# Kernel optimization log

Measured on AMD Instinct MI355X. Metric: run time of the kernel, lower is better.

## Reference

```python
import jax, jax.numpy as jnp
import numpy as np

EPS = 0.5  # energy-relaxation learning rate (epsilon in __init__)


def rho(s):
    return jnp.clip(s, 0.0, 1.0)


def setup_inputs() -> dict:
    key = jax.random.key(0)
    k_x, k_w1, k_w2 = jax.random.split(key, 3)
    B, I, H, O = 8192, 1024, 128, 1000
    x = jax.random.uniform(k_x, (B, I), dtype=jnp.float32)
    hidden0 = jnp.zeros((B, H), dtype=jnp.float32)
    output0 = jnp.zeros((B, O), dtype=jnp.float32)
    b_in = jnp.zeros((I,), dtype=jnp.float32)
    b_h = jnp.zeros((H,), dtype=jnp.float32)
    b_o = jnp.zeros((O,), dtype=jnp.float32)
    # xavier_uniform: U(-a, a), a = sqrt(6 / (fan_in + fan_out))
    a1 = np.sqrt(6.0 / (I + H)).astype(np.float32)
    a2 = np.sqrt(6.0 / (H + O)).astype(np.float32)
    W1 = jax.random.uniform(k_w1, (I, H), minval=-a1, maxval=a1, dtype=jnp.float32)
    W2 = jax.random.uniform(k_w2, (H, O), minval=-a2, maxval=a2, dtype=jnp.float32)
    return {"x": x, "hidden0": hidden0, "output0": output0,
            "b_in": b_in, "b_h": b_h, "b_o": b_o,
            "W1": W1, "W2": W2, "n_iterations": 30}


def reference(x, hidden0, output0, b_in, b_h, b_o, W1, W2, n_iterations):
    # Hopfield-style energy summed over the batch (beta=0 / free phase):
    # E = 0.5*sum rho(s)^2 - sum rho(s).b - sum rho(pre) W rho(post)
    def energy(h, o):
        rx, rh, ro = rho(x), rho(h), rho(o)
        sq = 0.5 * ((rx * rx).sum() + (rh * rh).sum() + (ro * ro).sum())
        lin = -(rx @ b_in).sum() - (rh @ b_h).sum() - (ro @ b_o).sum()
        quad = -jnp.einsum('bi,ih,bh->', rx, W1, rh) \
               - jnp.einsum('bh,ho,bo->', rh, W2, ro)
        return sq + lin + quad

    grad_e = jax.grad(energy, argnums=(0, 1))

    def step(carry, _):
        h, o = carry
        gh, go = grad_e(h, o)
        h = jnp.clip(h - EPS * gh, 0.0, 1.0)
        o = jnp.clip(o - EPS * go, 0.0, 1.0)
        return (h, o), None

    (h, o), _ = jax.lax.scan(step, (hidden0, output0), None, length=n_iterations)
    return jax.nn.log_softmax(o, axis=1)
```

## Files before the change

### kernel.cpp

```cpp
#include <hip/hip_runtime.h>
#include <hip/hip_bf16.h>

typedef __bf16 bf16_t;
typedef __bf16 bf16x4_t __attribute__((ext_vector_type(4)));
typedef __bf16 bf16x8 __attribute__((ext_vector_type(8)));
typedef float f32x16 __attribute__((ext_vector_type(16)));

#define EPS 0.5f
#define MFMA32(a, b, c) __builtin_amdgcn_mfma_f32_32x32x16_bf16(a, b, c, 0, 0, 0)

__device__ __forceinline__ int oswz(int row, int kbyte) {
  return (row << 11) + (kbyte ^ ((row & 15) << 4));
}
__device__ __forceinline__ int hswz(int row, int jbyte) {
  return (row << 8) + (jbyte ^ ((row & 15) << 4));
}

__global__ __launch_bounds__(256) void prep_weights(
    const float* __restrict__ W1, const float* __restrict__ W2,
    bf16_t* __restrict__ W1t, bf16_t* __restrict__ W2B, bf16_t* __restrict__ W2T) {
  int idx = blockIdx.x * 256 + threadIdx.x;
  if (idx < 131072) {
    { int j = idx >> 10, i = idx & 1023; W1t[idx] = (bf16_t)W1[i * 128 + j]; }
    { int e = idx & 7, l = (idx >> 3) & 63, s = (idx >> 9) & 63, jt = idx >> 15;
      int j = jt * 32 + (l & 31), k = s * 16 + (l >> 5) * 8 + e;
      W2B[idx] = (bf16_t)((k < 1000) ? W2[j * 1000 + k] : 0.f); }
    { int e = idx & 7, l = (idx >> 3) & 63, js = (idx >> 9) & 7, kt = idx >> 12;
      int k = kt * 32 + (l & 31), j = js * 16 + (l >> 5) * 8 + e;
      W2T[idx] = (bf16_t)((k < 1000) ? W2[j * 1000 + k] : 0.f); }
  }
}

__global__ __launch_bounds__(256) void gemm_A(
    const float* __restrict__ x, const bf16_t* __restrict__ W1t,
    float* __restrict__ A) {
  int lane = threadIdx.x & 63, w = threadIdx.x >> 6;
  int row0 = blockIdx.x * 64;
  int mt = w & 1, np = (w >> 1) * 2;
  f32x16 acc0 = {}, acc1 = {};
  int ar = row0 + mt * 32 + (lane & 31);
  int kg = (lane >> 5) * 8;
  const float* xrow = x + (size_t)ar * 1024 + kg;
  const bf16_t* b0 = W1t + ((np * 32 + (lane & 31)) << 10) + kg;
  const bf16_t* b1 = W1t + (((np + 1) * 32 + (lane & 31)) << 10) + kg;
#pragma unroll 4
  for (int ks = 0; ks < 64; ++ks) {
    float xv[8];
    *(float4*)&xv[0] = *(const float4*)(xrow + ks * 16);
    *(float4*)&xv[4] = *(const float4*)(xrow + ks * 16 + 4);
    bf16x8 a;
#pragma unroll
    for (int i = 0; i < 8; ++i) a[i] = (bf16_t)xv[i];
    bf16x8 f0 = *(const bf16x8*)(b0 + ks * 16);
    bf16x8 f1 = *(const bf16x8*)(b1 + ks * 16);
    acc0 = MFMA32(a, f0, acc0);
    acc1 = MFMA32(a, f1, acc1);
  }
#pragma unroll
  for (int reg = 0; reg < 16; ++reg) {
    int r = mt * 32 + (reg & 3) + 8 * (reg >> 2) + 4 * (lane >> 5);
    A[(size_t)(row0 + r) * 128 + np * 32 + (lane & 31)] = acc0[reg];
    A[(size_t)(row0 + r) * 128 + (np + 1) * 32 + (lane & 31)] = acc1[reg];
  }
}

__global__ __launch_bounds__(1024, 4) void eqprop(
    const float* __restrict__ h0, const float* __restrict__ o0,
    const float* __restrict__ b_h, const float* __restrict__ b_o,
    const float* __restrict__ A, const bf16_t* __restrict__ W2B,
    const bf16_t* __restrict__ W2T, const int* __restrict__ nit,
    float* __restrict__ out) {
  __shared__ __align__(16) char ob[2][65536];
  __shared__ __align__(16) char hb[2][8192];
  __shared__ float bo_lds[1024];

  const int tid = threadIdx.x, lane = tid & 63, w = tid >> 6;
  const int lo = lane & 31, hi = lane >> 5;
  const int row0 = blockIdx.x * 32;

  for (int idx = tid; idx < 8192; idx += 1024) {
    int r = idx >> 8, k4 = (idx & 255) * 4;
    bf16x4_t v4 = {};
    if (k4 < 1000) {
      float4 v = *(const float4*)(o0 + (size_t)(row0 + r) * 1000 + k4);
      v4[0] = (bf16_t)v.x; v4[1] = (bf16_t)v.y; v4[2] = (bf16_t)v.z; v4[3] = (bf16_t)v.w;
    }
    *(bf16x4_t*)(&ob[0][0] + oswz(r, k4 * 2)) = v4;
  }
  {
    int idx = tid;
    if (idx < 1024) {
      int r = idx >> 5, j4 = (idx & 31) * 4;
      float4 v = *(const float4*)(h0 + (size_t)(row0 + r) * 128 + j4);
      bf16x4_t v4;
      v4[0] = (bf16_t)v.x; v4[1] = (bf16_t)v.y; v4[2] = (bf16_t)v.z; v4[3] = (bf16_t)v.w;
      *(bf16x4_t*)(&hb[0][0] + hswz(r, j4 * 2)) = v4;
    }
  }
  bo_lds[tid] = (tid < 1000) ? b_o[tid] : 0.f;

  const int T = nit[0];
  int p = 0;
  __syncthreads();

  if (w < 4) {
    const int jt = w;
    const bf16_t* WB = W2B + (size_t)jt * 64 * 512 + lane * 8;
    bf16x8 wres[16];
#pragma unroll
    for (int s = 0; s < 16; ++s) wres[s] = *(const bf16x8*)(WB + s * 512);
    const bf16_t* WS = WB + 16 * 512;

    for (int t = 0; t < T; ++t) {
      const char* op = &ob[p][0];
      f32x16 acc = {};
#pragma unroll
      for (int s = 0; s < 16; ++s) {
        bf16x8 of = *(const bf16x8*)(op + oswz(lo, s * 32 + hi * 16));
        acc = MFMA32(wres[s], of, acc);
      }
#pragma unroll 1
      for (int c = 0; c < 12; ++c) {
        bf16x8 w0 = *(const bf16x8*)(WS + (c * 4 + 0) * 512);
        bf16x8 w1 = *(const bf16x8*)(WS + (c * 4 + 1) * 512);
        bf16x8 w2 = *(const bf16x8*)(WS + (c * 4 + 2) * 512);
        bf16x8 w3 = *(const bf16x8*)(WS + (c * 4 + 3) * 512);
        int s0 = (16 + c * 4) * 32 + hi * 16;
        bf16x8 f0 = *(const bf16x8*)(op + oswz(lo, s0));
        bf16x8 f1 = *(const bf16x8*)(op + oswz(lo, s0 + 32));
        bf16x8 f2 = *(const bf16x8*)(op + oswz(lo, s0 + 64));
        bf16x8 f3 = *(const bf16x8*)(op + oswz(lo, s0 + 96));
        acc = MFMA32(w0, f0, acc);
        acc = MFMA32(w1, f1, acc);
        acc = MFMA32(w2, f2, acc);
        acc = MFMA32(w3, f3, acc);
      }
      const char* hp = &hb[p][0];
      char* hn = &hb[p ^ 1][0];
#pragma unroll
      for (int q = 0; q < 4; ++q) {
        int jb = jt * 32 + q * 8 + 4 * hi;
        float av[4], bh[4];
        *(float4*)av = *(const float4*)(A + (size_t)(row0 + lo) * 128 + jb);
        *(float4*)bh = *(const float4*)(b_h + jb);
        bf16x4_t hv4 = *(const bf16x4_t*)(hp + hswz(lo, jb * 2));
        bf16x4_t hn4;
#pragma unroll
        for (int r = 0; r < 4; ++r) {
          float hv = (float)hv4[r];
          float rp = (hv == 0.f || hv == 1.f) ? 0.5f : 1.f;
          float nv = hv - EPS * rp * (hv - bh[r] - av[r] - acc[q * 4 + r]);
          hn4[r] = (bf16_t)fminf(fmaxf(nv, 0.f), 1.f);
        }
        *(bf16x4_t*)(hn + hswz(lo, jb * 2)) = hn4;
      }
      __syncthreads();
      p ^= 1;
    }
  } else {
    const int wd = w - 4;
    const int kt0 = (wd < 8) ? wd * 3 : 24 + (wd - 8) * 2;
    const int nkt = (wd < 8) ? 3 : 2;
    const bf16_t* WT = W2T + (size_t)kt0 * 8 * 512 + lane * 8;
    bf16x8 wres[12];
#pragma unroll
    for (int f = 0; f < 12; ++f) wres[f] = *(const bf16x8*)(WT + f * 512);

    for (int t = 0; t < T; ++t) {
      const char* hp = &hb[p][0];
      const char* op = &ob[p][0];
      char* on = &ob[p ^ 1][0];

#pragma unroll 1
      for (int kl = 0; kl < nkt; ++kl) {
        f32x16 acc = {};
        if (kl == 0) {
#pragma unroll
          for (int js = 0; js < 8; ++js) {
            bf16x8 hf = *(const bf16x8*)(hp + hswz(lo, js * 32 + hi * 16));
            acc = MFMA32(wres[js], hf, acc);
          }
        } else if (kl == 1) {
          bf16x8 s0 = *(const bf16x8*)(WT + 12 * 512);
          bf16x8 s1 = *(const bf16x8*)(WT + 13 * 512);
          bf16x8 s2 = *(const bf16x8*)(WT + 14 * 512);
          bf16x8 s3 = *(const bf16x8*)(WT + 15 * 512);
#pragma unroll
          for (int js = 0; js < 4; ++js) {
            bf16x8 hf = *(const bf16x8*)(hp + hswz(lo, js * 32 + hi * 16));
            acc = MFMA32(wres[8 + js], hf, acc);
          }
          {
            bf16x8 h4 = *(const bf16x8*)(hp + hswz(lo, 4 * 32 + hi * 16));
            bf16x8 h5 = *(const bf16x8*)(hp + hswz(lo, 5 * 32 + hi * 16));
            bf16x8 h6 = *(const bf16x8*)(hp + hswz(lo, 6 * 32 + hi * 16));
            bf16x8 h7 = *(const bf16x8*)(hp + hswz(lo, 7 * 32 + hi * 16));
            acc = MFMA32(s0, h4, acc);
            acc = MFMA32(s1, h5, acc);
            acc = MFMA32(s2, h6, acc);
            acc = MFMA32(s3, h7, acc);
          }
        } else {
          const bf16_t* WK = WT + 16 * 512;
          bf16x8 s0 = *(const bf16x8*)(WK + 0 * 512);
          bf16x8 s1 = *(const bf16x8*)(WK + 1 * 512);
          bf16x8 s2 = *(const bf16x8*)(WK + 2 * 512);
          bf16x8 s3 = *(const bf16x8*)(WK + 3 * 512);
#pragma unroll
          for (int js = 0; js < 4; ++js) {
            bf16x8 hf = *(const bf16x8*)(hp + hswz(lo, js * 32 + hi * 16));
            acc = MFMA32((js == 0) ? s0 : (js == 1) ? s1 : (js == 2) ? s2 : s3,
                         hf, acc);
          }
          bf16x8 s4 = *(const bf16x8*)(WK + 4 * 512);
          bf16x8 s5 = *(const bf16x8*)(WK + 5 * 512);
          bf16x8 s6 = *(const bf16x8*)(WK + 6 * 512);
          bf16x8 s7 = *(const bf16x8*)(WK + 7 * 512);
#pragma unroll
          for (int js = 4; js < 8; ++js) {
            bf16x8 hf = *(const bf16x8*)(hp + hswz(lo, js * 32 + hi * 16));
            acc = MFMA32((js == 4) ? s4 : (js == 5) ? s5 : (js == 6) ? s6 : s7,
                         hf, acc);
          }
        }
        int kt = kt0 + kl;
#pragma unroll
        for (int q = 0; q < 4; ++q) {
          int kb = kt * 32 + q * 8 + 4 * hi;
          float bo[4];
          *(float4*)bo = *(const float4*)(bo_lds + kb);
          bf16x4_t ov4 = *(const bf16x4_t*)(op + oswz(lo, kb * 2));
          bf16x4_t on4;
#pragma unroll
          for (int r = 0; r < 4; ++r) {
            float ov = (float)ov4[r];
            float rp = (ov == 0.f || ov == 1.f) ? 0.5f : 1.f;
            float nv = ov - EPS * rp * (ov - bo[r] - acc[q * 4 + r]);
            on4[r] = (bf16_t)fminf(fmaxf(nv, 0.f), 1.f);
          }
          *(bf16x4_t*)(on + oswz(lo, kb * 2)) = on4;
        }
      }
      __syncthreads();
      p ^= 1;
    }
  }
  __syncthreads();

  const char* of = &ob[p][0];
  for (int r = w * 2; r < w * 2 + 2; ++r) {
    float m = -1e30f;
    for (int k = lane; k < 1000; k += 64)
      m = fmaxf(m, (float)*(const bf16_t*)(of + oswz(r, k * 2)));
#pragma unroll
    for (int s = 32; s > 0; s >>= 1) m = fmaxf(m, __shfl_xor(m, s));
    float sum = 0.f;
    for (int k = lane; k < 1000; k += 64)
      sum += expf((float)*(const bf16_t*)(of + oswz(r, k * 2)) - m);
#pragma unroll
    for (int s = 32; s > 0; s >>= 1) sum += __shfl_xor(sum, s);
    float lse = m + logf(sum);
    for (int k = lane; k < 1000; k += 64)
      out[(size_t)(row0 + r) * 1000 + k] =
          (float)*(const bf16_t*)(of + oswz(r, k * 2)) - lse;
  }
}

extern "C" void kernel_launch(void* const* d_in, const int* in_sizes, int n_in,
                              void* d_out, int out_size, void* d_ws, size_t ws_size,
                              hipStream_t stream) {
  const float* x   = (const float*)d_in[0];
  const float* h0  = (const float*)d_in[1];
  const float* o0  = (const float*)d_in[2];
  const float* b_h = (const float*)d_in[4];
  const float* b_o = (const float*)d_in[5];
  const float* W1  = (const float*)d_in[6];
  const float* W2  = (const float*)d_in[7];
  const int*   nit = (const int*)d_in[8];
  float* out = (float*)d_out;

  char* ws = (char*)d_ws;
  float*  A   = (float*)ws;
  bf16_t* W1t = (bf16_t*)(ws + 4194304);
  bf16_t* W2B = (bf16_t*)(ws + 4194304 + 262144);
  bf16_t* W2T = (bf16_t*)(ws + 4194304 + 524288);

  prep_weights<<<512, 256, 0, stream>>>(W1, W2, W1t, W2B, W2T);
  gemm_A<<<128, 256, 0, stream>>>(x, W1t, A);
  eqprop<<<256, 1024, 0, stream>>>(h0, o0, b_h, b_o, A, W2B, W2T, nit, out);
}
```

Baseline: 227.0 us.

## Repack LDS state into MFMA-fragment layout and rebalance waves to 768 threads

Replaces the XOR-swizzled row-major LDS buffers for the output and hidden states with a layout that matches the MFMA fragment order, so each lane reads a contiguous 16-byte fragment with a simple offset. The output-update waves drop from 12 to 8, each owning 4 k-tiles with software-pipelined (double-buffered) streaming weight loads, and the block size drops from 1024 to 768. The A+b_h term is hoisted out of the iteration loop into registers, and the update math is rewritten with FMAs. The risks are higher register pressure per wave, fewer waves to hide latency, and a slower scalar-by-scalar initial fill of LDS.

```diff
diff --git a/kernel.cpp b/kernel.cpp
--- a/kernel.cpp
+++ b/kernel.cpp
@@ -8,13 +8,6 @@
 
 #define EPS 0.5f
 #define MFMA32(a, b, c) __builtin_amdgcn_mfma_f32_32x32x16_bf16(a, b, c, 0, 0, 0)
-
-__device__ __forceinline__ int oswz(int row, int kbyte) {
-  return (row << 11) + (kbyte ^ ((row & 15) << 4));
-}
-__device__ __forceinline__ int hswz(int row, int jbyte) {
-  return (row << 8) + (jbyte ^ ((row & 15) << 4));
-}
 
 __global__ __launch_bounds__(256) void prep_weights(
     const float* __restrict__ W1, const float* __restrict__ W2,
@@ -64,40 +57,33 @@
   }
 }
 
-__global__ __launch_bounds__(1024, 4) void eqprop(
+__global__ __launch_bounds__(768, 3) void eqprop(
     const float* __restrict__ h0, const float* __restrict__ o0,
     const float* __restrict__ b_h, const float* __restrict__ b_o,
     const float* __restrict__ A, const bf16_t* __restrict__ W2B,
     const bf16_t* __restrict__ W2T, const int* __restrict__ nit,
     float* __restrict__ out) {
-  __shared__ __align__(16) char ob[2][65536];
-  __shared__ __align__(16) char hb[2][8192];
+  __shared__ __align__(16) char o_raw[131072];
+  __shared__ __align__(16) char h_raw[16384];
   __shared__ float bo_lds[1024];
 
   const int tid = threadIdx.x, lane = tid & 63, w = tid >> 6;
   const int lo = lane & 31, hi = lane >> 5;
   const int row0 = blockIdx.x * 32;
 
-  for (int idx = tid; idx < 8192; idx += 1024) {
-    int r = idx >> 8, k4 = (idx & 255) * 4;
-    bf16x4_t v4 = {};
-    if (k4 < 1000) {
-      float4 v = *(const float4*)(o0 + (size_t)(row0 + r) * 1000 + k4);
-      v4[0] = (bf16_t)v.x; v4[1] = (bf16_t)v.y; v4[2] = (bf16_t)v.z; v4[3] = (bf16_t)v.w;
-    }
-    *(bf16x4_t*)(&ob[0][0] + oswz(r, k4 * 2)) = v4;
-  }
-  {
-    int idx = tid;
-    if (idx < 1024) {
-      int r = idx >> 5, j4 = (idx & 31) * 4;
-      float4 v = *(const float4*)(h0 + (size_t)(row0 + r) * 128 + j4);
-      bf16x4_t v4;
-      v4[0] = (bf16_t)v.x; v4[1] = (bf16_t)v.y; v4[2] = (bf16_t)v.z; v4[3] = (bf16_t)v.w;
-      *(bf16x4_t*)(&hb[0][0] + hswz(r, j4 * 2)) = v4;
-    }
-  }
-  bo_lds[tid] = (tid < 1000) ? b_o[tid] : 0.f;
+  for (int idx = tid; idx < 32768; idx += 768) {
+    int b = idx >> 10, k = idx & 1023;
+    float v = (k < 1000) ? o0[(size_t)(row0 + b) * 1000 + k] : 0.f;
+    int ad = ((k >> 4) << 10) + ((((k >> 3) & 1) << 5) + b) * 16 + ((k & 7) << 1);
+    *(bf16_t*)(o_raw + ad) = (bf16_t)v;
+  }
+  for (int idx = tid; idx < 4096; idx += 768) {
+    int b = idx >> 7, j = idx & 127;
+    int ad = ((j >> 4) << 10) + ((((j >> 3) & 1) << 5) + b) * 16 + ((j & 7) << 1);
+    *(bf16_t*)(h_raw + ad) = (bf16_t)h0[(size_t)(row0 + b) * 128 + j];
+  }
+  for (int idx = tid; idx < 1024; idx += 768)
+    bo_lds[idx] = (idx < 1000) ? b_o[idx] : 0.f;
 
   const int T = nit[0];
   int p = 0;
@@ -105,164 +91,173 @@
 
   if (w < 4) {
     const int jt = w;
-    const bf16_t* WB = W2B + (size_t)jt * 64 * 512 + lane * 8;
+    const bf16_t* WB = W2B + (size_t)jt * 32768 + lane * 8;
+#define CW(s) (*(const bf16x8*)(WB + (s) * 512))
     bf16x8 wres[16];
 #pragma unroll
-    for (int s = 0; s < 16; ++s) wres[s] = *(const bf16x8*)(WB + s * 512);
-    const bf16_t* WS = WB + 16 * 512;
+    for (int s = 0; s < 16; ++s) wres[s] = CW(s);
+    float uh[16];
+#pragma unroll
+    for (int q = 0; q < 4; ++q) {
+      int jb = jt * 32 + q * 8 + 4 * hi;
+      float4 a4 = *(const float4*)(A + (size_t)(row0 + lo) * 128 + jb);
+      float4 b4 = *(const float4*)(b_h + jb);
+      uh[q * 4 + 0] = a4.x + b4.x; uh[q * 4 + 1] = a4.y + b4.y;
+      uh[q * 4 + 2] = a4.z + b4.z; uh[q * 4 + 3] = a4.w + b4.w;
+    }
+    const char* obase = o_raw + lane * 16;
+    const char* hrd_b = h_raw + lo * 16 + hi * 8;
+    char* hwr_b = h_raw + lo * 16 + hi * 8;
 
     for (int t = 0; t < T; ++t) {
-      const char* op = &ob[p][0];
+      const char* obP = obase + (p << 16);
+#define OF(s) (*(const bf16x8*)(obP + (s) * 1024))
       f32x16 acc = {};
 #pragma unroll
-      for (int s = 0; s < 16; ++s) {
-        bf16x8 of = *(const bf16x8*)(op + oswz(lo, s * 32 + hi * 16));
-        acc = MFMA32(wres[s], of, acc);
+      for (int s = 0; s < 16; ++s) acc = MFMA32(wres[s], OF(s), acc);
+      bf16x8 cs0[4], cs1[4];
+      cs0[0] = CW(16); cs0[1] = CW(17); cs0[2] = CW(18); cs0[3] = CW(19);
+#pragma unroll
+      for (int c = 0; c < 12; ++c) {
+        const int s0 = 16 + c * 4;
+        if ((c & 1) == 0) {
+          if (c < 11) {
+            cs1[0] = CW(s0 + 4); cs1[1] = CW(s0 + 5);
+            cs1[2] = CW(s0 + 6); cs1[3] = CW(s0 + 7);
+          }
+          acc = MFMA32(cs0[0], OF(s0 + 0), acc);
+          acc = MFMA32(cs0[1], OF(s0 + 1), acc);
+          acc = MFMA32(cs0[2], OF(s0 + 2), acc);
+          acc = MFMA32(cs0[3], OF(s0 + 3), acc);
+        } else {
+          if (c < 11) {
+            cs0[0] = CW(s0 + 4); cs0[1] = CW(s0 + 5);
+            cs0[2] = CW(s0 + 6); cs0[3] = CW(s0 + 7);
+          }
+          acc = MFMA32(cs1[0], OF(s0 + 0), acc);
+          acc = MFMA32(cs1[1], OF(s0 + 1), acc);
+          acc = MFMA32(cs1[2], OF(s0 + 2), acc);
+          acc = MFMA32(cs1[3], OF(s0 + 3), acc);
+        }
       }
-#pragma unroll 1
-      for (int c = 0; c < 12; ++c) {
-        bf16x8 w0 = *(const bf16x8*)(WS + (c * 4 + 0) * 512);
-        bf16x8 w1 = *(const bf16x8*)(WS + (c * 4 + 1) * 512);
-        bf16x8 w2 = *(const bf16x8*)(WS + (c * 4 + 2) * 512);
-        bf16x8 w3 = *(const bf16x8*)(WS + (c * 4 + 3) * 512);
-        int s0 = (16 + c * 4) * 32 + hi * 16;
-        bf16x8 f0 = *(const bf16x8*)(op + oswz(lo, s0));
-        bf16x8 f1 = *(const bf16x8*)(op + oswz(lo, s0 + 32));
-        bf16x8 f2 = *(const bf16x8*)(op + oswz(lo, s0 + 64));
-        bf16x8 f3 = *(const bf16x8*)(op + oswz(lo, s0 + 96));
-        acc = MFMA32(w0, f0, acc);
-        acc = MFMA32(w1, f1, acc);
-        acc = MFMA32(w2, f2, acc);
-        acc = MFMA32(w3, f3, acc);
-      }
-      const char* hp = &hb[p][0];
-      char* hn = &hb[p ^ 1][0];
+      const char* hrd = hrd_b + (p << 13);
+      char* hwr = hwr_b + ((p ^ 1) << 13);
 #pragma unroll
       for (int q = 0; q < 4; ++q) {
-        int jb = jt * 32 + q * 8 + 4 * hi;
-        float av[4], bh[4];
-        *(float4*)av = *(const float4*)(A + (size_t)(row0 + lo) * 128 + jb);
-        *(float4*)bh = *(const float4*)(b_h + jb);
-        bf16x4_t hv4 = *(const bf16x4_t*)(hp + hswz(lo, jb * 2));
+        const int boff = (jt * 2 + (q >> 1)) * 1024 + (q & 1) * 512;
+        bf16x4_t hv4 = *(const bf16x4_t*)(hrd + boff);
         bf16x4_t hn4;
 #pragma unroll
         for (int r = 0; r < 4; ++r) {
           float hv = (float)hv4[r];
-          float rp = (hv == 0.f || hv == 1.f) ? 0.5f : 1.f;
-          float nv = hv - EPS * rp * (hv - bh[r] - av[r] - acc[q * 4 + r]);
+          float tie = __builtin_fmaf(hv, hv, -hv);
+          float st = (tie == 0.f) ? 0.25f : 0.5f;
+          float nv = __builtin_fmaf(-st, hv - uh[q * 4 + r] - acc[q * 4 + r], hv);
           hn4[r] = (bf16_t)fminf(fmaxf(nv, 0.f), 1.f);
         }
-        *(bf16x4_t*)(hn + hswz(lo, jb * 2)) = hn4;
+        *(bf16x4_t*)(hwr + boff) = hn4;
       }
       __syncthreads();
       p ^= 1;
     }
   } else {
-    const int wd = w - 4;
-    const int kt0 = (wd < 8) ? wd * 3 : 24 + (wd - 8) * 2;
-    const int nkt = (wd < 8) ? 3 : 2;
-    const bf16_t* WT = W2T + (size_t)kt0 * 8 * 512 + lane * 8;
-    bf16x8 wres[12];
-#pragma unroll
-    for (int f = 0; f < 12; ++f) wres[f] = *(const bf16x8*)(WT + f * 512);
+    const int wd4 = (w - 4) * 4;
+    const bf16_t* WT = W2T + lane * 8;
+#define DW(kt, js) (*(const bf16x8*)(WT + (size_t)((kt) * 8 + (js)) * 512))
+#define DLOAD(dst, kt) { dst[0] = DW(kt, 4); dst[1] = DW(kt, 5); \
+                         dst[2] = DW(kt, 6); dst[3] = DW(kt, 7); }
+    bf16x8 wr[4][4];
+#pragma unroll
+    for (int i = 0; i < 4; ++i)
+#pragma unroll
+      for (int js = 0; js < 4; ++js) wr[i][js] = DW(wd4 + i, js);
+
+    const char* hbase = h_raw + lane * 16;
+    const char* ord_b = o_raw + lo * 16 + hi * 8;
+    char* owr_b = o_raw + lo * 16 + hi * 8;
 
     for (int t = 0; t < T; ++t) {
-      const char* hp = &hb[p][0];
-      const char* op = &ob[p][0];
-      char* on = &ob[p ^ 1][0];
-
-#pragma unroll 1
-      for (int kl = 0; kl < nkt; ++kl) {
+      const char* hbP = hbase + (p << 13);
+      bf16x8 hf[8];
+#pragma unroll
+      for (int js = 0; js < 8; ++js)
+        hf[js] = *(const bf16x8*)(hbP + js * 1024);
+      const char* ord = ord_b + (p << 16);
+      char* owr = owr_b + ((p ^ 1) << 16);
+
+      bf16x8 sw0[4], sw1[4];
+      DLOAD(sw0, wd4);
+#pragma unroll
+      for (int i = 0; i < 4; ++i) {
+        const int kt = wd4 + i;
         f32x16 acc = {};
-        if (kl == 0) {
-#pragma unroll
-          for (int js = 0; js < 8; ++js) {
-            bf16x8 hf = *(const bf16x8*)(hp + hswz(lo, js * 32 + hi * 16));
-            acc = MFMA32(wres[js], hf, acc);
-          }
-        } else if (kl == 1) {
-          bf16x8 s0 = *(const bf16x8*)(WT + 12 * 512);
-          bf16x8 s1 = *(const bf16x8*)(WT + 13 * 512);
-          bf16x8 s2 = *(const bf16x8*)(WT + 14 * 512);
-          bf16x8 s3 = *(const bf16x8*)(WT + 15 * 512);
-#pragma unroll
-          for (int js = 0; js < 4; ++js) {
-            bf16x8 hf = *(const bf16x8*)(hp + hswz(lo, js * 32 + hi * 16));
-            acc = MFMA32(wres[8 + js], hf, acc);
-          }
-          {
-            bf16x8 h4 = *(const bf16x8*)(hp + hswz(lo, 4 * 32 + hi * 16));
-            bf16x8 h5 = *(const bf16x8*)(hp + hswz(lo, 5 * 32 + hi * 16));
-            bf16x8 h6 = *(const bf16x8*)(hp + hswz(lo, 6 * 32 + hi * 16));
-            bf16x8 h7 = *(const bf16x8*)(hp + hswz(lo, 7 * 32 + hi * 16));
-            acc = MFMA32(s0, h4, acc);
-            acc = MFMA32(s1, h5, acc);
-            acc = MFMA32(s2, h6, acc);
-            acc = MFMA32(s3, h7, acc);
-          }
+        if ((i & 1) == 0) {
+          if (i < 3) DLOAD(sw1, kt + 1);
+          acc = MFMA32(wr[i][0], hf[0], acc);
+          acc = MFMA32(wr[i][1], hf[1], acc);
+          acc = MFMA32(wr[i][2], hf[2], acc);
+          acc = MFMA32(wr[i][3], hf[3], acc);
+          acc = MFMA32(sw0[0], hf[4], acc);
+          acc = MFMA32(sw0[1], hf[5], acc);
+          acc = MFMA32(sw0[2], hf[6], acc);
+          acc = MFMA32(sw0[3], hf[7], acc);
         } else {
-          const bf16_t* WK = WT + 16 * 512;
-          bf16x8 s0 = *(const bf16x8*)(WK + 0 * 512);
-          bf16x8 s1 = *(const bf16x8*)(WK + 1 * 512);
-          bf16x8 s2 = *(const bf16x8*)(WK + 2 * 512);
-          bf16x8 s3 = *(const bf16x8*)(WK + 3 * 512);
-#pragma unroll
-          for (int js = 0; js < 4; ++js) {
-            bf16x8 hf = *(const bf16x8*)(hp + hswz(lo, js * 32 + hi * 16));
-            acc = MFMA32((js == 0) ? s0 : (js == 1) ? s1 : (js == 2) ? s2 : s3,
-                         hf, acc);
-          }
-          bf16x8 s4 = *(const bf16x8*)(WK + 4 * 512);
-          bf16x8 s5 = *(const bf16x8*)(WK + 5 * 512);
-          bf16x8 s6 = *(const bf16x8*)(WK + 6 * 512);
-          bf16x8 s7 = *(const bf16x8*)(WK + 7 * 512);
-#pragma unroll
-          for (int js = 4; js < 8; ++js) {
-            bf16x8 hf = *(const bf16x8*)(hp + hswz(lo, js * 32 + hi * 16));
-            acc = MFMA32((js == 4) ? s4 : (js == 5) ? s5 : (js == 6) ? s6 : s7,
-                         hf, acc);
-          }
-        }
-        int kt = kt0 + kl;
+          if (i < 3) DLOAD(sw0, kt + 1);
+          acc = MFMA32(wr[i][0], hf[0], acc);
+          acc = MFMA32(wr[i][1], hf[1], acc);
+          acc = MFMA32(wr[i][2], hf[2], acc);
+          acc = MFMA32(wr[i][3], hf[3], acc);
+          acc = MFMA32(sw1[0], hf[4], acc);
+          acc = MFMA32(sw1[1], hf[5], acc);
+          acc = MFMA32(sw1[2], hf[6], acc);
+          acc = MFMA32(sw1[3], hf[7], acc);
+        }
 #pragma unroll
         for (int q = 0; q < 4; ++q) {
-          int kb = kt * 32 + q * 8 + 4 * hi;
-          float bo[4];
-          *(float4*)bo = *(const float4*)(bo_lds + kb);
-          bf16x4_t ov4 = *(const bf16x4_t*)(op + oswz(lo, kb * 2));
+          const int boff = (kt * 2 + (q >> 1)) * 1024 + (q & 1) * 512;
+          float bov[4];
+          *(float4*)bov = *(const float4*)(bo_lds + kt * 32 + q * 8 + 4 * hi);
+          bf16x4_t ov4 = *(const bf16x4_t*)(ord + boff);
           bf16x4_t on4;
 #pragma unroll
           for (int r = 0; r < 4; ++r) {
             float ov = (float)ov4[r];
-            float rp = (ov == 0.f || ov == 1.f) ? 0.5f : 1.f;
-            float nv = ov - EPS * rp * (ov - bo[r] - acc[q * 4 + r]);
+            float u = bov[r] + acc[q * 4 + r];
+            float tie = __builtin_fmaf(ov, ov, -ov);
+            float st = (tie == 0.f) ? 0.25f : 0.5f;
+            float nv = __builtin_fmaf(-st, ov - u, ov);
             on4[r] = (bf16_t)fminf(fmaxf(nv, 0.f), 1.f);
           }
-          *(bf16x4_t*)(on + oswz(lo, kb * 2)) = on4;
+          *(bf16x4_t*)(owr + boff) = on4;
         }
       }
       __syncthreads();
       p ^= 1;
     }
   }
-  __syncthreads();
-
-  const char* of = &ob[p][0];
-  for (int r = w * 2; r < w * 2 + 2; ++r) {
+
+  const char* of = o_raw + (p << 16);
+  for (int row = w; row < 32; row += 12) {
     float m = -1e30f;
-    for (int k = lane; k < 1000; k += 64)
-      m = fmaxf(m, (float)*(const bf16_t*)(of + oswz(r, k * 2)));
+    for (int k = lane; k < 1000; k += 64) {
+      int ad = ((k >> 4) << 10) + ((((k >> 3) & 1) << 5) + row) * 16 + ((k & 7) << 1);
+      m = fmaxf(m, (float)*(const bf16_t*)(of + ad));
+    }
 #pragma unroll
     for (int s = 32; s > 0; s >>= 1) m = fmaxf(m, __shfl_xor(m, s));
     float sum = 0.f;
-    for (int k = lane; k < 1000; k += 64)
-      sum += expf((float)*(const bf16_t*)(of + oswz(r, k * 2)) - m);
+    for (int k = lane; k < 1000; k += 64) {
+      int ad = ((k >> 4) << 10) + ((((k >> 3) & 1) << 5) + row) * 16 + ((k & 7) << 1);
+      sum += expf((float)*(const bf16_t*)(of + ad) - m);
+    }
 #pragma unroll
     for (int s = 32; s > 0; s >>= 1) sum += __shfl_xor(sum, s);
     float lse = m + logf(sum);
-    for (int k = lane; k < 1000; k += 64)
-      out[(size_t)(row0 + r) * 1000 + k] =
-          (float)*(const bf16_t*)(of + oswz(r, k * 2)) - lse;
+    for (int k = lane; k < 1000; k += 64) {
+      int ad = ((k >> 4) << 10) + ((((k >> 3) & 1) << 5) + row) * 16 + ((k & 7) << 1);
+      out[(size_t)(row0 + row) * 1000 + k] =
+          (float)*(const bf16_t*)(of + ad) - lse;
+    }
   }
 }
 
@@ -287,5 +282,5 @@
 
   prep_weights<<<512, 256, 0, stream>>>(W1, W2, W1t, W2B, W2T);
   gemm_A<<<128, 256, 0, stream>>>(x, W1t, A);
-  eqprop<<<256, 1024, 0, stream>>>(h0, o0, b_h, b_o, A, W2B, W2T, nit, out);
-}
+  eqprop<<<256, 768, 0, stream>>>(h0, o0, b_h, b_o, A, W2B, W2T, nit, out);
+}
```

New measurement: 537.5 us. 137% more time.
